# Performance work log

Hardware: AMD Instinct MI355X
Metric: run time of the kernel (lower is better)

## Reference

```python
import jax, jax.numpy as jnp
import numpy as np

N_CELL, N_DRUG = 8192, 4096


def setup_inputs() -> dict:
    key = jax.random.key(0)
    adj = jax.random.uniform(key, (N_CELL, N_DRUG), dtype=jnp.float32)
    return {"adj": adj}


def reference(adj):
    # Degree normalizations with +1 self-loop smoothing, as in the torch module.
    d_x = (jnp.sum(adj, axis=1) + 1.0) ** -0.5  # [N_CELL]
    d_y = (jnp.sum(adj, axis=0) + 1.0) ** -0.5  # [N_DRUG]

    # diag(d_x) @ adj @ diag(d_y) == row/col broadcast scaling (same math, O(n^2)).
    agg_cell_lp = d_x[:, None] * adj * d_y[None, :]          # [N_CELL, N_DRUG]
    agg_drug_lp = d_y[:, None] * adj.T * d_x[None, :]        # [N_DRUG, N_CELL]

    d_c = (jnp.sum(adj, axis=1) + 1.0) ** -1.0               # [N_CELL]
    self_cell_lp = jnp.diag(d_c + 1.0)                       # [N_CELL, N_CELL]
    d_d = (jnp.sum(adj, axis=0) + 1.0) ** -1.0               # [N_DRUG]
    self_drug_lp = jnp.diag(d_d + 1.0)                       # [N_DRUG, N_DRUG]

    return (agg_cell_lp, agg_drug_lp, self_cell_lp, self_drug_lp)
```

## Files before the change

kernel.cpp:

```cpp
#include <hip/hip_runtime.h>

#define N_CELL 8192
#define N_DRUG 4096

typedef float f32x4 __attribute__((ext_vector_type(4)));

static constexpr size_t OFF1 = (size_t)N_CELL * N_DRUG;
static constexpr size_t OFF2 = 2ull * N_CELL * N_DRUG;
static constexpr size_t OFF3 = OFF2 + (size_t)N_CELL * N_CELL;
static constexpr size_t FILL_F4 = ((size_t)N_CELL * N_CELL + (size_t)N_DRUG * N_DRUG) / 4;

#define SUM_BLOCKS 512
#define FILL_BLOCKS 1280
#define MEGA_BLOCKS (SUM_BLOCKS + FILL_BLOCKS)
static constexpr size_t FILL_PER_BLOCK = FILL_F4 / FILL_BLOCKS;

__global__ __launch_bounds__(256, 8) void mega_kernel(const float* __restrict__ adj,
                                                      float* __restrict__ rowsum,
                                                      float* __restrict__ colsum,
                                                      float* __restrict__ fill_base) {
    int b = blockIdx.x;
    int tid = threadIdx.x;
    if (b >= SUM_BLOCKS) {
        f32x4 z = {0.f, 0.f, 0.f, 0.f};
        f32x4* p = reinterpret_cast<f32x4*>(fill_base) + (size_t)(b - SUM_BLOCKS) * FILL_PER_BLOCK;
#pragma unroll 4
        for (size_t i = tid; i < FILL_PER_BLOCK; i += 256) {
            __builtin_nontemporal_store(z, p + i);
        }
        return;
    }
    __shared__ float part[64][65];
    int cb = b & 3, rb = b >> 2;
    int c0 = cb * 1024, r0 = rb * 64;
    const f32x4* ap = reinterpret_cast<const f32x4*>(adj + (size_t)r0 * N_DRUG + c0) + tid;
    f32x4 cacc = {0.f, 0.f, 0.f, 0.f};
#pragma unroll 4
    for (int r = 0; r < 64; ++r) {
        f32x4 v = ap[(size_t)r * (N_DRUG / 4)];
        cacc += v;
        float h = (v.x + v.y) + (v.z + v.w);
        h += __shfl_down(h, 1, 64);
        h += __shfl_down(h, 2, 64);
        if ((tid & 3) == 0) part[r][tid >> 2] = h;
    }
    __syncthreads();
    if (tid < 64) {
        float s = 0.f;
#pragma unroll 8
        for (int j = 0; j < 64; ++j) s += part[tid][j];
        atomicAdd(&rowsum[r0 + tid], s);
    }
    int c = c0 + tid * 4;
    atomicAdd(&colsum[c + 0], cacc.x);
    atomicAdd(&colsum[c + 1], cacc.y);
    atomicAdd(&colsum[c + 2], cacc.z);
    atomicAdd(&colsum[c + 3], cacc.w);
}

#define SCALE_TILES 2048
#define DIAG_BLOCKS 48
__global__ __launch_bounds__(256, 8) void scale_kernel(const float* __restrict__ adj,
                                                       const float* __restrict__ rowsum,
                                                       const float* __restrict__ colsum,
                                                       float* __restrict__ out) {
    int tid = threadIdx.x;
    int b = blockIdx.x;
    if (b >= SCALE_TILES) {
        int idx = (b - SCALE_TILES) * 256 + tid;
        if (idx < N_CELL) {
            out[OFF2 + (size_t)idx * (N_CELL + 1)] = 1.0f / (rowsum[idx] + 1.0f) + 1.0f;
        } else {
            int k = idx - N_CELL;
            out[OFF3 + (size_t)k * (N_DRUG + 1)] = 1.0f / (colsum[k] + 1.0f) + 1.0f;
        }
        return;
    }
    __shared__ float lds[64][69];
    int tx = tid & 15;
    int ty = tid >> 4;
    int c0 = (b & 31) * 128;
    int r0 = (b >> 5) * 128;
    float* aggd = out + OFF1;
#pragma unroll 1
    for (int s = 0; s < 4; ++s) {
        int cc = c0 + (s & 1) * 64;
        int rr0 = r0 + (s >> 1) * 64;
        f32x4 cs = *reinterpret_cast<const f32x4*>(colsum + cc + tx * 4);
        f32x4 dy;
        dy.x = rsqrtf(cs.x + 1.0f);
        dy.y = rsqrtf(cs.y + 1.0f);
        dy.z = rsqrtf(cs.z + 1.0f);
        dy.w = rsqrtf(cs.w + 1.0f);
#pragma unroll
        for (int q = 0; q < 4; ++q) {
            int rr = q * 16 + ty;
            int r = rr0 + rr;
            float dx = rsqrtf(rowsum[r] + 1.0f);
            f32x4 v = *reinterpret_cast<const f32x4*>(adj + (size_t)r * N_DRUG + cc + tx * 4);
            f32x4 o = v * dx;
            o *= dy;
            __builtin_nontemporal_store(
                o, reinterpret_cast<f32x4*>(out + (size_t)r * N_DRUG + cc + tx * 4));
            lds[rr][tx * 4 + 0] = o.x;
            lds[rr][tx * 4 + 1] = o.y;
            lds[rr][tx * 4 + 2] = o.z;
            lds[rr][tx * 4 + 3] = o.w;
        }
        __syncthreads();
#pragma unroll
        for (int q = 0; q < 4; ++q) {
            int dr = q * 16 + ty;
            f32x4 o;
            o.x = lds[tx * 4 + 0][dr];
            o.y = lds[tx * 4 + 1][dr];
            o.z = lds[tx * 4 + 2][dr];
            o.w = lds[tx * 4 + 3][dr];
            __builtin_nontemporal_store(
                o, reinterpret_cast<f32x4*>(aggd + (size_t)(cc + dr) * N_CELL + rr0 + tx * 4));
        }
        __syncthreads();
    }
}

extern "C" void kernel_launch(void* const* d_in, const int* in_sizes, int n_in,
                              void* d_out, int out_size, void* d_ws, size_t ws_size,
                              hipStream_t stream) {
    const float* adj = (const float*)d_in[0];
    float* out = (float*)d_out;
    float* rowsum = (float*)d_ws;
    float* colsum = rowsum + N_CELL;

    (void)hipMemsetAsync(d_ws, 0, (N_CELL + N_DRUG) * sizeof(float), stream);

    mega_kernel<<<MEGA_BLOCKS, 256, 0, stream>>>(adj, rowsum, colsum, out + OFF2);
    scale_kernel<<<SCALE_TILES + DIAG_BLOCKS, 256, 0, stream>>>(adj, rowsum, colsum, out);
}
```

Measured before the change: 152.7 us.

## Transpose full 128x128 tile through swizzled LDS in one pass

```diff
diff --git a/kernel.cpp b/kernel.cpp
--- a/kernel.cpp
+++ b/kernel.cpp
@@ -60,10 +60,15 @@
 
 #define SCALE_TILES 2048
 #define DIAG_BLOCKS 48
-__global__ __launch_bounds__(256, 8) void scale_kernel(const float* __restrict__ adj,
-                                                       const float* __restrict__ rowsum,
-                                                       const float* __restrict__ colsum,
-                                                       float* __restrict__ out) {
+
+__device__ __forceinline__ int swz(int r, int c) {
+    return c ^ ((r >> 2) & 31) ^ (c >> 5);
+}
+
+__global__ __launch_bounds__(256) void scale_kernel(const float* __restrict__ adj,
+                                                    const float* __restrict__ rowsum,
+                                                    const float* __restrict__ colsum,
+                                                    float* __restrict__ out) {
     int tid = threadIdx.x;
     int b = blockIdx.x;
     if (b >= SCALE_TILES) {
@@ -76,50 +81,50 @@
         }
         return;
     }
-    __shared__ float lds[64][69];
-    int tx = tid & 15;
-    int ty = tid >> 4;
+    __shared__ float lds[128][128];
     int c0 = (b & 31) * 128;
     int r0 = (b >> 5) * 128;
+
+    int tx = tid & 31;
+    int ty = tid >> 5;
+    f32x4 cs = *reinterpret_cast<const f32x4*>(colsum + c0 + tx * 4);
+    f32x4 dy;
+    dy.x = rsqrtf(cs.x + 1.0f);
+    dy.y = rsqrtf(cs.y + 1.0f);
+    dy.z = rsqrtf(cs.z + 1.0f);
+    dy.w = rsqrtf(cs.w + 1.0f);
+    int cbase = tx * 4;
+#pragma unroll 4
+    for (int i = 0; i < 16; ++i) {
+        int rr = i * 8 + ty;
+        int r = r0 + rr;
+        float dx = rsqrtf(rowsum[r] + 1.0f);
+        const f32x4* src = reinterpret_cast<const f32x4*>(adj + (size_t)r * N_DRUG + c0 + cbase);
+        f32x4 v = __builtin_nontemporal_load(src);
+        f32x4 o = v * dx;
+        o *= dy;
+        __builtin_nontemporal_store(
+            o, reinterpret_cast<f32x4*>(out + (size_t)r * N_DRUG + c0 + cbase));
+        lds[rr][swz(rr, cbase + 0)] = o.x;
+        lds[rr][swz(rr, cbase + 1)] = o.y;
+        lds[rr][swz(rr, cbase + 2)] = o.z;
+        lds[rr][swz(rr, cbase + 3)] = o.w;
+    }
+    __syncthreads();
+
     float* aggd = out + OFF1;
-#pragma unroll 1
-    for (int s = 0; s < 4; ++s) {
-        int cc = c0 + (s & 1) * 64;
-        int rr0 = r0 + (s >> 1) * 64;
-        f32x4 cs = *reinterpret_cast<const f32x4*>(colsum + cc + tx * 4);
-        f32x4 dy;
-        dy.x = rsqrtf(cs.x + 1.0f);
-        dy.y = rsqrtf(cs.y + 1.0f);
-        dy.z = rsqrtf(cs.z + 1.0f);
-        dy.w = rsqrtf(cs.w + 1.0f);
-#pragma unroll
-        for (int q = 0; q < 4; ++q) {
-            int rr = q * 16 + ty;
-            int r = rr0 + rr;
-            float dx = rsqrtf(rowsum[r] + 1.0f);
-            f32x4 v = *reinterpret_cast<const f32x4*>(adj + (size_t)r * N_DRUG + cc + tx * 4);
-            f32x4 o = v * dx;
-            o *= dy;
-            __builtin_nontemporal_store(
-                o, reinterpret_cast<f32x4*>(out + (size_t)r * N_DRUG + cc + tx * 4));
-            lds[rr][tx * 4 + 0] = o.x;
-            lds[rr][tx * 4 + 1] = o.y;
-            lds[rr][tx * 4 + 2] = o.z;
-            lds[rr][tx * 4 + 3] = o.w;
-        }
-        __syncthreads();
-#pragma unroll
-        for (int q = 0; q < 4; ++q) {
-            int dr = q * 16 + ty;
-            f32x4 o;
-            o.x = lds[tx * 4 + 0][dr];
-            o.y = lds[tx * 4 + 1][dr];
-            o.z = lds[tx * 4 + 2][dr];
-            o.w = lds[tx * 4 + 3][dr];
-            __builtin_nontemporal_store(
-                o, reinterpret_cast<f32x4*>(aggd + (size_t)(cc + dr) * N_CELL + rr0 + tx * 4));
-        }
-        __syncthreads();
+    int tx2 = tid & 31;
+    int dj = tid >> 5;
+#pragma unroll 4
+    for (int i = 0; i < 16; ++i) {
+        int dd = i * 8 + dj;
+        f32x4 o;
+        o.x = lds[tx2 * 4 + 0][swz(tx2 * 4 + 0, dd)];
+        o.y = lds[tx2 * 4 + 1][swz(tx2 * 4 + 1, dd)];
+        o.z = lds[tx2 * 4 + 2][swz(tx2 * 4 + 2, dd)];
+        o.w = lds[tx2 * 4 + 3][swz(tx2 * 4 + 3, dd)];
+        __builtin_nontemporal_store(
+            o, reinterpret_cast<f32x4*>(aggd + (size_t)(c0 + dd) * N_CELL + r0 + tx2 * 4));
     }
 }
 
```

After: 171.5 us. +12.3%, slower.

## Reshape scale kernel to 512-thread 128-row tiles with hoisted row scales

Applied to the files above, without the earlier changes.

```diff
diff --git a/kernel.cpp b/kernel.cpp
--- a/kernel.cpp
+++ b/kernel.cpp
@@ -58,16 +58,16 @@
     atomicAdd(&colsum[c + 3], cacc.w);
 }
 
-#define SCALE_TILES 2048
-#define DIAG_BLOCKS 48
-__global__ __launch_bounds__(256, 8) void scale_kernel(const float* __restrict__ adj,
+#define DIAG_BLOCKS 24
+#define SCALE_BLOCKS 1024
+__global__ __launch_bounds__(512, 8) void scale_kernel(const float* __restrict__ adj,
                                                        const float* __restrict__ rowsum,
                                                        const float* __restrict__ colsum,
                                                        float* __restrict__ out) {
     int tid = threadIdx.x;
     int b = blockIdx.x;
-    if (b >= SCALE_TILES) {
-        int idx = (b - SCALE_TILES) * 256 + tid;
+    if (b < DIAG_BLOCKS) {
+        int idx = b * 512 + tid;
         if (idx < N_CELL) {
             out[OFF2 + (size_t)idx * (N_CELL + 1)] = 1.0f / (rowsum[idx] + 1.0f) + 1.0f;
         } else {
@@ -76,16 +76,27 @@
         }
         return;
     }
-    __shared__ float lds[64][69];
+    __shared__ float lds[128][65];
+    int t = b - DIAG_BLOCKS;
+    int rt = t >> 4;
+    int ci = t & 15;
+    int r0 = rt * 128;
+    int cg = ci * 256;
+    float* aggd = out + OFF1;
+
     int tx = tid & 15;
     int ty = tid >> 4;
-    int c0 = (b & 31) * 128;
-    int r0 = (b >> 5) * 128;
-    float* aggd = out + OFF1;
+    int tx2 = tid & 31;
+    int dj = tid >> 5;
+
+    float dx0 = rsqrtf(rowsum[r0 + 0 * 32 + ty] + 1.0f);
+    float dx1 = rsqrtf(rowsum[r0 + 1 * 32 + ty] + 1.0f);
+    float dx2 = rsqrtf(rowsum[r0 + 2 * 32 + ty] + 1.0f);
+    float dx3 = rsqrtf(rowsum[r0 + 3 * 32 + ty] + 1.0f);
+
 #pragma unroll 1
     for (int s = 0; s < 4; ++s) {
-        int cc = c0 + (s & 1) * 64;
-        int rr0 = r0 + (s >> 1) * 64;
+        int cc = cg + s * 64;
         f32x4 cs = *reinterpret_cast<const f32x4*>(colsum + cc + tx * 4);
         f32x4 dy;
         dy.x = rsqrtf(cs.x + 1.0f);
@@ -93,10 +104,10 @@
         dy.z = rsqrtf(cs.z + 1.0f);
         dy.w = rsqrtf(cs.w + 1.0f);
 #pragma unroll
-        for (int q = 0; q < 4; ++q) {
-            int rr = q * 16 + ty;
-            int r = rr0 + rr;
-            float dx = rsqrtf(rowsum[r] + 1.0f);
+        for (int i = 0; i < 4; ++i) {
+            int rr = i * 32 + ty;
+            int r = r0 + rr;
+            float dx = (i == 0) ? dx0 : (i == 1) ? dx1 : (i == 2) ? dx2 : dx3;
             f32x4 v = *reinterpret_cast<const f32x4*>(adj + (size_t)r * N_DRUG + cc + tx * 4);
             f32x4 o = v * dx;
             o *= dy;
@@ -109,15 +120,15 @@
         }
         __syncthreads();
 #pragma unroll
-        for (int q = 0; q < 4; ++q) {
-            int dr = q * 16 + ty;
+        for (int i = 0; i < 4; ++i) {
+            int dd = i * 16 + dj;
             f32x4 o;
-            o.x = lds[tx * 4 + 0][dr];
-            o.y = lds[tx * 4 + 1][dr];
-            o.z = lds[tx * 4 + 2][dr];
-            o.w = lds[tx * 4 + 3][dr];
+            o.x = lds[tx2 * 4 + 0][dd];
+            o.y = lds[tx2 * 4 + 1][dd];
+            o.z = lds[tx2 * 4 + 2][dd];
+            o.w = lds[tx2 * 4 + 3][dd];
             __builtin_nontemporal_store(
-                o, reinterpret_cast<f32x4*>(aggd + (size_t)(cc + dr) * N_CELL + rr0 + tx * 4));
+                o, reinterpret_cast<f32x4*>(aggd + (size_t)(cc + dd) * N_CELL + r0 + tx2 * 4));
         }
         __syncthreads();
     }
@@ -134,5 +145,5 @@
     (void)hipMemsetAsync(d_ws, 0, (N_CELL + N_DRUG) * sizeof(float), stream);
 
     mega_kernel<<<MEGA_BLOCKS, 256, 0, stream>>>(adj, rowsum, colsum, out + OFF2);
-    scale_kernel<<<SCALE_TILES + DIAG_BLOCKS, 256, 0, stream>>>(adj, rowsum, colsum, out);
+    scale_kernel<<<DIAG_BLOCKS + SCALE_BLOCKS, 512, 0, stream>>>(adj, rowsum, colsum, out);
 }
```

Measured after the change: 159.7 us. 4.6% more time.
